# Kernel tuning notes

Measured on AMD Instinct MI355X. Metric: run time of the kernel, lower is better.

Reference implementation:

```python
import jax, jax.numpy as jnp
import numpy as np

NUM_EMBEDDINGS = 1024
EMBEDDING_SIZE = 256
COMMITMENT_COST = 0.25


def setup_inputs() -> dict:
    key = jax.random.key(0)
    kx, kw = jax.random.split(key)
    x = jax.random.normal(kx, (16, EMBEDDING_SIZE, 64, 64), dtype=jnp.float32)
    # nn.Embedding init: uniform(-1/K, 1/K)
    w = jax.random.uniform(kw, (NUM_EMBEDDINGS, EMBEDDING_SIZE), dtype=jnp.float32,
                           minval=-1.0 / NUM_EMBEDDINGS, maxval=1.0 / NUM_EMBEDDINGS)
    return {"x": x, "w": w}


def reference(x, w):
    # x: [B, C, H, W] -> NHWC
    xh = jnp.transpose(x, (0, 2, 3, 1))  # [B, H, W, D]
    B, H, W, D = xh.shape
    x_flat = xh.reshape(-1, D)  # [N, D]
    distances = (jnp.sum(x_flat * x_flat, axis=1, keepdims=True)
                 + jnp.sum(w * w, axis=1)
                 - 2.0 * (x_flat @ w.T))  # [N, K]
    indices_flat = jnp.argmin(distances, axis=1)  # [N]
    quantized = w[indices_flat].reshape(B, H, W, D)
    indices = indices_flat.reshape(B, H, W)[:, None, :, :]  # [B,1,H,W]
    # training-mode losses
    e_latent_loss = jnp.mean((jax.lax.stop_gradient(quantized) - xh) ** 2)
    q_latent_loss = jnp.mean((quantized - jax.lax.stop_gradient(xh)) ** 2)
    loss = q_latent_loss + COMMITMENT_COST * e_latent_loss
    # straight-through estimator
    quantized = xh + jax.lax.stop_gradient(quantized - xh)
    quantized = jnp.transpose(quantized, (0, 3, 1, 2))  # back to NCHW
    return quantized, indices, loss
```

## Files before the change

### kernel.cpp

```cpp
#include <hip/hip_runtime.h>
#include <math.h>

#define NUM_K 1024
#define DIM 256
#define HW 4096
#define NPIX 65536
#define QELEMS 16777216
#define MAX_FLAGS 16384

typedef short bf16x8 __attribute__((ext_vector_type(8)));
typedef float f32x4 __attribute__((ext_vector_type(4)));

__device__ __forceinline__ unsigned short f32_to_bf16_rne(float f) {
    unsigned int u = __float_as_uint(f);
    unsigned int r = u + 0x7FFFu + ((u >> 16) & 1u);
    return (unsigned short)(r >> 16);
}

__device__ __forceinline__ void merge3(float& a1d, int& a1i, float& a2d, int& a2i, float& a3d,
                                       float b1d, int b1i, float b2d, int b2i, float b3d) {
    bool bf = (b1d < a1d) || (b1d == a1d && b1i < a1i);
    float r1d = bf ? b1d : a1d; int r1i = bf ? b1i : a1i;
    float n2d = bf ? b2d : a2d; int n2i = bf ? b2i : a2i;
    float o1d = bf ? a1d : b1d; int o1i = bf ? a1i : b1i;
    bool k2 = (n2d < o1d) || (n2d == o1d && n2i < o1i);
    float r2d = k2 ? n2d : o1d; int r2i = k2 ? n2i : o1i;
    float sm3 = bf ? b3d : a3d;
    float o2d = bf ? a2d : b2d;
    float r3d = k2 ? fminf(sm3, o1d) : fminf(n2d, o2d);
    a1d = r1d; a1i = r1i; a2d = r2d; a2i = r2i; a3d = r3d;
}

__device__ __forceinline__ float np_sumsq_256(const float* __restrict__ p, long stride) {
    float blk0 = 0.f, blk1 = 0.f;
#pragma unroll
    for (int h = 0; h < 2; ++h) {
        const float* base = p + (long)h * 128 * stride;
        float s[16];
#pragma unroll
        for (int L = 0; L < 16; ++L) {
            float a0 = base[(long)(L)       * stride]; a0 = __fmul_rn(a0, a0);
            float a1 = base[(long)(16 + L)  * stride]; a1 = __fmul_rn(a1, a1);
            float a2 = base[(long)(32 + L)  * stride]; a2 = __fmul_rn(a2, a2);
            float a3 = base[(long)(48 + L)  * stride]; a3 = __fmul_rn(a3, a3);
            float a4 = base[(long)(64 + L)  * stride]; a4 = __fmul_rn(a4, a4);
            float a5 = base[(long)(80 + L)  * stride]; a5 = __fmul_rn(a5, a5);
            float a6 = base[(long)(96 + L)  * stride]; a6 = __fmul_rn(a6, a6);
            float a7 = base[(long)(112 + L) * stride]; a7 = __fmul_rn(a7, a7);
            float t1 = __fadd_rn(a0, a1);
            float t2 = __fadd_rn(a2, a3);
            float t3 = __fadd_rn(a4, a5);
            float t4 = __fadd_rn(a6, a7);
            s[L] = __fadd_rn(__fadd_rn(t1, t2), __fadd_rn(t3, t4));
        }
        float c0 = __fadd_rn(s[0], s[8]);
        float c1 = __fadd_rn(s[1], s[9]);
        float c2 = __fadd_rn(s[2], s[10]);
        float c3 = __fadd_rn(s[3], s[11]);
        float c4 = __fadd_rn(s[4], s[12]);
        float c5 = __fadd_rn(s[5], s[13]);
        float c6 = __fadd_rn(s[6], s[14]);
        float c7 = __fadd_rn(s[7], s[15]);
        float d0 = __fadd_rn(c0, c4);
        float d1 = __fadd_rn(c1, c5);
        float d2 = __fadd_rn(c2, c6);
        float d3 = __fadd_rn(c3, c7);
        float e0 = __fadd_rn(d0, d2);
        float e1 = __fadd_rn(d1, d3);
        float r  = __fadd_rn(e0, e1);
        if (h == 0) blk0 = r; else blk1 = r;
    }
    return __fadd_rn(blk0, blk1);
}

__global__ __launch_bounds__(256) void k_wsq(const float* __restrict__ w, float* __restrict__ wsq) {
    int k = blockIdx.x * 256 + threadIdx.x;
    if (k < NUM_K) wsq[k] = np_sumsq_256(w + (long)k * DIM, 1);
}

__global__ __launch_bounds__(256) void k_xsq(const float* __restrict__ x, float* __restrict__ xsq) {
    int n = blockIdx.x * 256 + threadIdx.x;
    int b = n >> 12, hw = n & 4095;
    xsq[n] = np_sumsq_256(x + (long)b * DIM * HW + hw, HW);
}

__global__ __launch_bounds__(1024)
void k_wtrans(const float* __restrict__ w, float* __restrict__ wtr) {
    int d = blockIdx.x;
    int k = threadIdx.x;
    wtr[(long)d * NUM_K + k] = w[(long)k * DIM + d];
}

__global__ __launch_bounds__(256)
void k_wfrag(const float* __restrict__ w, short* __restrict__ whi) {
    int id = blockIdx.x * 256 + threadIdx.x;
    int code = id >> 5;
    int c = id & 31;
    const float* src = w + (long)code * DIM + c * 8;
    bf16x8 vh;
#pragma unroll
    for (int j = 0; j < 8; ++j) vh[j] = (short)f32_to_bf16_rne(src[j]);
    int fl = ((c & 3) << 4) | (code & 15);
    long addr = ((((long)(code >> 4) * 8 + (c >> 2)) * 64 + fl) * 8);
    *(bf16x8*)(whi + addr) = vh;
}

#define A_SLOT(ks,m,fl) ((((ks)*4+(m))*64+(fl))*8)

__global__ __launch_bounds__(256, 2)
void k_argmin_mfma(const float* __restrict__ x,
                   const short* __restrict__ whi,
                   const float* __restrict__ wsq, float* __restrict__ xsq,
                   int* __restrict__ idx,
                   int4* __restrict__ pairf, int* __restrict__ paircnt,
                   int* __restrict__ fullf, int* __restrict__ fullcnt) {
    __shared__ short ahi[8 * 4 * 64 * 8];
    __shared__ float xpart[4 * 16 * 64];
    __shared__ float xsq_s[64];
    __shared__ float cd1[4][64], cd2[4][64], cd3[4][64];
    __shared__ int   ci1[4][64], ci2[4][64];

    const int t = threadIdx.x;
    const int lane = t & 63;
    const int q = t >> 6;
    const int tile = blockIdx.x;
    const int b = tile >> 6;
    const int hw0 = (tile & 63) * 64;
    const long px0 = (long)tile * 64;
    const float* xb = x + (long)b * (DIM * HW) + hw0 + lane;

    {
        float tmp[16], part[16];
#pragma unroll
        for (int i = 0; i < 8; ++i) {
            int c = q * 8 + i;
            float v[8];
#pragma unroll
            for (int jj = 0; jj < 8; ++jj) v[jj] = xb[(long)(c * 8 + jj) * HW];
            bf16x8 vh;
#pragma unroll
            for (int jj = 0; jj < 8; ++jj) vh[jj] = (short)f32_to_bf16_rne(v[jj]);
            int slot = A_SLOT(c >> 2, lane >> 4, ((c & 3) << 4) | (lane & 15));
            *(bf16x8*)(ahi + slot) = vh;
            const int kp = i >> 1;
#pragma unroll
            for (int jj = 0; jj < 8; ++jj) {
                int L = ((i & 1) << 3) | jj;
                float a = __fmul_rn(v[jj], v[jj]);
                if (kp == 0) tmp[L] = a;
                else if (kp == 1) part[L] = __fadd_rn(tmp[L], a);
                else if (kp == 2) tmp[L] = a;
                else part[L] = __fadd_rn(part[L], __fadd_rn(tmp[L], a));
            }
        }
#pragma unroll
        for (int L = 0; L < 16; ++L) xpart[(q * 16 + L) * 64 + lane] = part[L];
    }
    __syncthreads();

    if (t < 64) {
        float blk[2];
#pragma unroll
        for (int h = 0; h < 2; ++h) {
            float s[16];
#pragma unroll
            for (int L = 0; L < 16; ++L)
                s[L] = __fadd_rn(xpart[((2 * h) * 16 + L) * 64 + t],
                                 xpart[((2 * h + 1) * 16 + L) * 64 + t]);
            float c0 = __fadd_rn(s[0], s[8]);
            float c1 = __fadd_rn(s[1], s[9]);
            float c2 = __fadd_rn(s[2], s[10]);
            float c3 = __fadd_rn(s[3], s[11]);
            float c4 = __fadd_rn(s[4], s[12]);
            float c5 = __fadd_rn(s[5], s[13]);
            float c6 = __fadd_rn(s[6], s[14]);
            float c7 = __fadd_rn(s[7], s[15]);
            float d0 = __fadd_rn(c0, c4);
            float d1 = __fadd_rn(c1, c5);
            float d2 = __fadd_rn(c2, c6);
            float d3 = __fadd_rn(c3, c7);
            float e0 = __fadd_rn(d0, d2);
            float e1 = __fadd_rn(d1, d3);
            blk[h] = __fadd_rn(e0, e1);
        }
        float v = __fadd_rn(blk[0], blk[1]);
        xsq_s[t] = v;
        xsq[px0 + t] = v;
    }
    __syncthreads();

#pragma unroll
    for (int s = 0; s < 2; ++s) {
        const int ct0 = s * 32 + q * 8;
        f32x4 acc[4][8];
#pragma unroll
        for (int m = 0; m < 4; ++m)
#pragma unroll
            for (int n = 0; n < 8; ++n) acc[m][n] = (f32x4){0.f, 0.f, 0.f, 0.f};

#define BADDR(i) ((((long)(ct0 + ((i) & 7)) * 8 + ((i) >> 3)) * 64 + lane) * 8)
        bf16x8 bring[4];
#pragma unroll
        for (int i = 0; i < 4; ++i) bring[i] = *(const bf16x8*)(whi + BADDR(i));

        bf16x8 ah[4];
#pragma unroll
        for (int i = 0; i < 64; ++i) {
            const int ks = i >> 3;
            const int n = i & 7;
            if (n == 0) {
#pragma unroll
                for (int m = 0; m < 4; ++m)
                    ah[m] = *(const bf16x8*)(ahi + A_SLOT(ks, m, lane));
            }
            bf16x8 bcur = bring[i & 3];
            if (i + 4 < 64) bring[i & 3] = *(const bf16x8*)(whi + BADDR(i + 4));
#pragma unroll
            for (int m = 0; m < 4; ++m)
                acc[m][n] = __builtin_amdgcn_mfma_f32_16x16x32_bf16(ah[m], bcur, acc[m][n], 0, 0, 0);
        }
#undef BADDR

        const int rbase = (lane >> 4) * 4;
        float s1v[4][4];
#pragma unroll
        for (int m = 0; m < 4; ++m)
#pragma unroll
            for (int r = 0; r < 4; ++r) s1v[m][r] = xsq_s[16 * m + rbase + r];

        float e1d[4][4], e2d[4][4], e3d[4][4];
        int   e1i[4][4], e2i[4][4];
#pragma unroll
        for (int m = 0; m < 4; ++m)
#pragma unroll
            for (int r = 0; r < 4; ++r) {
                e1d[m][r] = INFINITY; e2d[m][r] = INFINITY; e3d[m][r] = INFINITY;
                e1i[m][r] = 0; e2i[m][r] = 0;
            }

#pragma unroll
        for (int n = 0; n < 8; ++n) {
            int code = (ct0 + n) * 16 + (lane & 15);
            float wq = wsq[code];
#pragma unroll
            for (int m = 0; m < 4; ++m) {
#pragma unroll
                for (int r = 0; r < 4; ++r) {
                    float tt = __fadd_rn(s1v[m][r], wq);
                    float dist = __fmaf_rn(-2.0f, acc[m][n][r], tt);
                    bool c1 = dist < e1d[m][r];
                    bool c2 = dist < e2d[m][r];
                    bool c3 = dist < e3d[m][r];
                    float n3 = c2 ? e2d[m][r] : (c3 ? dist : e3d[m][r]);
                    float n2 = c1 ? e1d[m][r] : (c2 ? dist : e2d[m][r]);
                    int   j2 = c1 ? e1i[m][r] : (c2 ? code : e2i[m][r]);
                    float n1 = c1 ? dist : e1d[m][r];
                    int   j1 = c1 ? code : e1i[m][r];
                    e3d[m][r] = n3; e2d[m][r] = n2; e2i[m][r] = j2;
                    e1d[m][r] = n1; e1i[m][r] = j1;
                }
            }
        }

#pragma unroll
        for (int step = 1; step < 16; step <<= 1) {
#pragma unroll
            for (int m = 0; m < 4; ++m) {
#pragma unroll
                for (int r = 0; r < 4; ++r) {
                    float o1 = __shfl_xor(e1d[m][r], step);
                    int   p1 = __shfl_xor(e1i[m][r], step);
                    float o2 = __shfl_xor(e2d[m][r], step);
                    int   p2 = __shfl_xor(e2i[m][r], step);
                    float o3 = __shfl_xor(e3d[m][r], step);
                    merge3(e1d[m][r], e1i[m][r], e2d[m][r], e2i[m][r], e3d[m][r],
                           o1, p1, o2, p2, o3);
                }
            }
        }

        if ((lane & 15) == 0) {
#pragma unroll
            for (int m = 0; m < 4; ++m) {
#pragma unroll
                for (int r = 0; r < 4; ++r) {
                    int px = 16 * m + rbase + r;
                    if (s == 0) {
                        cd1[q][px] = e1d[m][r]; ci1[q][px] = e1i[m][r];
                        cd2[q][px] = e2d[m][r]; ci2[q][px] = e2i[m][r];
                        cd3[q][px] = e3d[m][r];
                    } else {
                        float a1 = cd1[q][px], a2 = cd2[q][px], a3 = cd3[q][px];
                        int   ai = ci1[q][px], aj = ci2[q][px];
                        merge3(a1, ai, a2, aj, a3,
                               e1d[m][r], e1i[m][r], e2d[m][r], e2i[m][r], e3d[m][r]);
                        cd1[q][px] = a1; ci1[q][px] = ai;
                        cd2[q][px] = a2; ci2[q][px] = aj;
                        cd3[q][px] = a3;
                    }
                }
            }
        }
    }
    __syncthreads();

    if (t < 64) {
        float d1 = cd1[0][t], d2 = cd2[0][t], d3 = cd3[0][t];
        int   i1 = ci1[0][t], i2 = ci2[0][t];
#pragma unroll
        for (int sq = 1; sq < 4; ++sq) {
            merge3(d1, i1, d2, i2, d3,
                   cd1[sq][t], ci1[sq][t], cd2[sq][t], ci2[sq][t], cd3[sq][t]);
        }
        const long n = px0 + t;
        idx[n] = i1;
        float m = d1 * 2.5e-6f;
        if (__fsub_rn(d3, d1) <= m) {
            int pos = atomicAdd(fullcnt, 1);
            if (pos < MAX_FLAGS) fullf[pos] = (int)n;
        } else if (__fsub_rn(d2, d1) <= m) {
            int pos = atomicAdd(paircnt, 1);
            if (pos < MAX_FLAGS) pairf[pos] = (int4){(int)n, i1, i2, 0};
        }
    }
}

__global__ __launch_bounds__(256, 2)
void k_argmin_valu(const float* __restrict__ x, const float* __restrict__ w,
                   const float* __restrict__ wsq, const float* __restrict__ xsq,
                   int* __restrict__ idx, int* __restrict__ fullf, int* __restrict__ fullcnt) {
    __shared__ float xs[64 * 257];
    __shared__ float sd1[4][64];
    __shared__ float sd2[4][64];
    __shared__ int   si1[4][64];

    const int t = threadIdx.x;
    const int p = t & 63;
    const int q = t >> 6;
    const long n0 = (long)blockIdx.x * 64;
    const int b = (int)(n0 >> 12);
    const int hw0 = (int)(n0 & 4095);
    const float* xb = x + (long)b * DIM * HW + hw0;

    for (int i = 0; i < 64; ++i) {
        int c = q * 64 + i;
        xs[p * 257 + c] = xb[(long)c * HW + p];
    }
    __syncthreads();

    const float* xrow = xs + p * 257;
    const float s1 = xsq[n0 + p];
    float d1 = INFINITY, d2 = INFINITY;
    int i1 = 0;
    const int kbase = q * 256;
    const float* wq = w + (long)kbase * DIM;
    const float* wsq_q = wsq + kbase;

    for (int kc = 0; kc < 256; kc += 8) {
        float acc[8] = {0.f, 0.f, 0.f, 0.f, 0.f, 0.f, 0.f, 0.f};
        const float* w0 = wq + (long)kc * DIM;
#pragma unroll 2
        for (int d = 0; d < DIM; d += 4) {
            float x0 = xrow[d + 0];
            float x1 = xrow[d + 1];
            float x2 = xrow[d + 2];
            float x3 = xrow[d + 3];
#pragma unroll
            for (int j = 0; j < 8; ++j) {
                const float4 wv = *reinterpret_cast<const float4*>(w0 + j * DIM + d);
                acc[j] = __fmaf_rn(x0, wv.x, acc[j]);
                acc[j] = __fmaf_rn(x1, wv.y, acc[j]);
                acc[j] = __fmaf_rn(x2, wv.z, acc[j]);
                acc[j] = __fmaf_rn(x3, wv.w, acc[j]);
            }
        }
#pragma unroll
        for (int j = 0; j < 8; ++j) {
            float tk = __fadd_rn(s1, wsq_q[kc + j]);
            float dist = __fsub_rn(tk, __fmul_rn(2.0f, acc[j]));
            if (dist < d1) { d2 = d1; d1 = dist; i1 = kbase + kc + j; }
            else if (dist < d2) { d2 = dist; }
        }
    }

    sd1[q][p] = d1; sd2[q][p] = d2; si1[q][p] = i1;
    __syncthreads();
    if (q == 0) {
        float bd1 = sd1[0][p], bd2 = sd2[0][p];
        int bi = si1[0][p];
#pragma unroll
        for (int j = 1; j < 4; ++j) {
            float a1 = sd1[j][p], a2 = sd2[j][p];
            int ai = si1[j][p];
            if (a1 < bd1) { bd2 = fminf(bd1, a2); bd1 = a1; bi = ai; }
            else { bd2 = fminf(bd2, fminf(a1, a2)); }
        }
        const long n = n0 + p;
        idx[n] = bi;
        if (__fsub_rn(bd2, bd1) <= bd1 * 6.0e-7f) {
            int pos = atomicAdd(fullcnt, 1);
            if (pos < MAX_FLAGS) fullf[pos] = (int)n;
        }
    }
}

__global__ __launch_bounds__(256)
void k_refine_pair(const float* __restrict__ x, const float* __restrict__ w,
                   const float* __restrict__ wsq, const float* __restrict__ xsq,
                   const int4* __restrict__ pairf, const int* __restrict__ paircnt,
                   int* __restrict__ idx) {
    int np = *paircnt;
    if (np > MAX_FLAGS) np = MAX_FLAGS;
    const int lane = threadIdx.x & 63;
    const int wv = threadIdx.x >> 6;
    for (int fi = blockIdx.x * 4 + wv; fi < np; fi += gridDim.x * 4) {
        int4 f = pairf[fi];
        int n = f.x, c1 = f.y, c2 = f.z;
        int b = n >> 12, hw = n & 4095;
        const float* xp = x + (long)b * (DIM * HW) + hw;
        double xd0 = (double)xp[(long)(lane * 4 + 0) * HW];
        double xd1 = (double)xp[(long)(lane * 4 + 1) * HW];
        double xd2 = (double)xp[(long)(lane * 4 + 2) * HW];
        double xd3 = (double)xp[(long)(lane * 4 + 3) * HW];
        const float4 w1 = *reinterpret_cast<const float4*>(w + (long)c1 * DIM + lane * 4);
        const float4 w2 = *reinterpret_cast<const float4*>(w + (long)c2 * DIM + lane * 4);
        double s1 = fma((double)w1.x, xd0, fma((double)w1.y, xd1,
                    fma((double)w1.z, xd2, (double)w1.w * xd3)));
        double s2 = fma((double)w2.x, xd0, fma((double)w2.y, xd1,
                    fma((double)w2.z, xd2, (double)w2.w * xd3)));
#pragma unroll
        for (int st = 1; st < 64; st <<= 1) {
            s1 += __shfl_xor(s1, st);
            s2 += __shfl_xor(s2, st);
        }
        if (lane == 0) {
            float xq = xsq[n];
            float dk1 = __fsub_rn(__fadd_rn(xq, wsq[c1]), __fmul_rn(2.0f, (float)s1));
            float dk2 = __fsub_rn(__fadd_rn(xq, wsq[c2]), __fmul_rn(2.0f, (float)s2));
            bool take2 = (dk2 < dk1) || (dk2 == dk1 && c2 < c1);
            idx[n] = take2 ? c2 : c1;
        }
    }
}

__global__ __launch_bounds__(1024)
void k_refine_full(const float* __restrict__ x, const float* __restrict__ wtr,
                   const float* __restrict__ wsq, const float* __restrict__ xsq,
                   const int* __restrict__ fullf, const int* __restrict__ fullcnt,
                   int* __restrict__ idx) {
    __shared__ float xsf[DIM][8];
    __shared__ int   np_s[8];
    __shared__ float s1_s[8];
    __shared__ float wd[16][8];
    __shared__ int   wi[16][8];

    int nf = *fullcnt;
    if (nf > MAX_FLAGS) nf = MAX_FLAGS;
    const int t = threadIdx.x;
    const int lane = t & 63;
    const int wid = t >> 6;

    for (int base = blockIdx.x * 8; base < nf; base += gridDim.x * 8) {
        __syncthreads();
        if (t < 8) {
            int fi = base + t;
            int n = fullf[fi < nf ? fi : (nf - 1)];
            np_s[t] = n;
            s1_s[t] = xsq[n];
        }
        __syncthreads();
#pragma unroll
        for (int e = t; e < 2048; e += 1024) {
            int p = e & 7, d = e >> 3;
            int n = np_s[p];
            xsf[d][p] = x[(long)(n >> 12) * (DIM * HW) + (long)d * HW + (n & 4095)];
        }
        __syncthreads();

        const float wq = wsq[t];
        double acc[8] = {0.0, 0.0, 0.0, 0.0, 0.0, 0.0, 0.0, 0.0};
#pragma unroll 4
        for (int d = 0; d < DIM; ++d) {
            double wk = (double)wtr[(long)d * NUM_K + t];
#pragma unroll
            for (int p = 0; p < 8; ++p) acc[p] = fma(wk, (double)xsf[d][p], acc[p]);
        }

        float dkv[8];
        int   kiv[8];
#pragma unroll
        for (int p = 0; p < 8; ++p) {
            dkv[p] = __fsub_rn(__fadd_rn(s1_s[p], wq), __fmul_rn(2.0f, (float)acc[p]));
            kiv[p] = t;
        }
#pragma unroll
        for (int step = 1; step < 64; step <<= 1) {
#pragma unroll
            for (int p = 0; p < 8; ++p) {
                float od = __shfl_xor(dkv[p], step);
                int   oi = __shfl_xor(kiv[p], step);
                if (od < dkv[p] || (od == dkv[p] && oi < kiv[p])) { dkv[p] = od; kiv[p] = oi; }
            }
        }
        if (lane == 0) {
#pragma unroll
            for (int p = 0; p < 8; ++p) { wd[wid][p] = dkv[p]; wi[wid][p] = kiv[p]; }
        }
        __syncthreads();
        if (t < 8) {
            float bd = wd[0][t];
            int   bi = wi[0][t];
#pragma unroll
            for (int sq = 1; sq < 16; ++sq) {
                float ad = wd[sq][t];
                int   ai = wi[sq][t];
                if (ad < bd || (ad == bd && ai < bi)) { bd = ad; bi = ai; }
            }
            if (base + t < nf) idx[np_s[t]] = bi;
        }
    }
}

__global__ __launch_bounds__(256, 2)
void k_quant(const float* __restrict__ x, const float* __restrict__ w,
             const int* __restrict__ idx, float* __restrict__ qout,
             float* __restrict__ iout, float* __restrict__ loss) {
    __shared__ float wrow[64 * 257];
    __shared__ int lidx[64];
    __shared__ float part[4];
    const int t = threadIdx.x;
    const long n0 = (long)blockIdx.x * 64;
    const int b = (int)(n0 >> 12), hw0 = (int)(n0 & 4095);

    if (t < 64) lidx[t] = idx[n0 + t];
    __syncthreads();
    for (int i = 0; i < 64; ++i) {
        wrow[i * 257 + t] = w[(long)lidx[i] * DIM + t];
    }
    if (t < 64) iout[n0 + t] = (float)lidx[t];
    __syncthreads();

    const int p = t & 63, cg = t >> 6;
    const float* xb = x + (long)b * DIM * HW + hw0;
    float* qb = qout + (long)b * DIM * HW + hw0;
    float lsum = 0.f;
    for (int i = 0; i < 64; ++i) {
        int c = cg * 64 + i;
        float qv = wrow[p * 257 + c];
        long off = (long)c * HW + p;
        float xv = xb[off];
        float diff = __fsub_rn(qv, xv);
        qb[off] = __fadd_rn(xv, diff);
        lsum = __fmaf_rn(diff, diff, lsum);
    }
#pragma unroll
    for (int off = 32; off; off >>= 1) lsum += __shfl_down(lsum, off);
    if ((t & 63) == 0) part[t >> 6] = lsum;
    __syncthreads();
    if (t == 0) {
        float tot = (part[0] + part[1]) + (part[2] + part[3]);
        atomicAdd(loss, tot * (1.25f / 16777216.f));
    }
}

extern "C" void kernel_launch(void* const* d_in, const int* in_sizes, int n_in,
                              void* d_out, int out_size, void* d_ws, size_t ws_size,
                              hipStream_t stream) {
    const float* x = (const float*)d_in[0];
    const float* w = (const float*)d_in[1];

    float* qout = (float*)d_out;
    float* iout = qout + QELEMS;
    float* loss = iout + NPIX;

    char* wp = (char*)d_ws;
    int*   idx     = (int*)wp;      wp += (size_t)NPIX * 4;
    float* wsq     = (float*)wp;    wp += (size_t)NUM_K * 4;
    float* xsq     = (float*)wp;    wp += (size_t)NPIX * 4;
    int4*  pairf   = (int4*)wp;     wp += (size_t)MAX_FLAGS * 16;
    int*   paircnt = (int*)wp;      wp += 256;
    int*   fullf   = (int*)wp;      wp += (size_t)MAX_FLAGS * 4;
    int*   fullcnt = (int*)wp;      wp += 256;
    float* wtr     = (float*)wp;    wp += (size_t)NUM_K * DIM * 4;
    short* whi     = (short*)wp;    wp += (size_t)NUM_K * DIM * 2;
    size_t need = (size_t)(wp - (char*)d_ws);

    hipMemsetAsync(loss, 0, sizeof(float), stream);
    hipMemsetAsync(paircnt, 0, sizeof(int), stream);
    hipMemsetAsync(fullcnt, 0, sizeof(int), stream);

    k_wsq<<<4, 256, 0, stream>>>(w, wsq);
    k_wtrans<<<DIM, 1024, 0, stream>>>(w, wtr);

    if (ws_size >= need) {
        k_wfrag<<<128, 256, 0, stream>>>(w, whi);
        k_argmin_mfma<<<1024, 256, 0, stream>>>(x, whi, wsq, xsq, idx,
                                                pairf, paircnt, fullf, fullcnt);
        k_refine_pair<<<2048, 256, 0, stream>>>(x, w, wsq, xsq, pairf, paircnt, idx);
    } else {
        k_xsq<<<NPIX / 256, 256, 0, stream>>>(x, xsq);
        k_argmin_valu<<<NPIX / 64, 256, 0, stream>>>(x, w, wsq, xsq, idx, fullf, fullcnt);
    }
    k_refine_full<<<512, 1024, 0, stream>>>(x, wtr, wsq, xsq, fullf, fullcnt, idx);
    k_quant<<<NPIX / 64, 256, 0, stream>>>(x, w, idx, qout, iout, loss);
}
```

Baseline: 239.7 us.

## Fuse codebook prep kernels and memsets; keep top-3 across both MFMA passes

```diff
diff --git a/kernel.cpp b/kernel.cpp
--- a/kernel.cpp
+++ b/kernel.cpp
@@ -73,36 +73,45 @@
     return __fadd_rn(blk0, blk1);
 }
 
-__global__ __launch_bounds__(256) void k_wsq(const float* __restrict__ w, float* __restrict__ wsq) {
-    int k = blockIdx.x * 256 + threadIdx.x;
-    if (k < NUM_K) wsq[k] = np_sumsq_256(w + (long)k * DIM, 1);
+__global__ __launch_bounds__(256)
+void k_prep(const float* __restrict__ w, float* __restrict__ wsq,
+            float* __restrict__ wtr, short* __restrict__ whi,
+            float* __restrict__ loss, int* __restrict__ paircnt, int* __restrict__ fullcnt) {
+    const int bk = blockIdx.x;
+    const int t = threadIdx.x;
+    if (bk < 128) {
+        int id = bk * 256 + t;
+        int code = id >> 5;
+        int c = id & 31;
+        const float* src = w + (long)code * DIM + c * 8;
+        bf16x8 vh;
+#pragma unroll
+        for (int j = 0; j < 8; ++j) vh[j] = (short)f32_to_bf16_rne(src[j]);
+        int fl = ((c & 3) << 4) | (code & 15);
+        long addr = ((((long)(code >> 4) * 8 + (c >> 2)) * 64 + fl) * 8);
+        *(bf16x8*)(whi + addr) = vh;
+    } else if (bk < 256) {
+        int d0 = (bk - 128) * 2;
+#pragma unroll
+        for (int dd = 0; dd < 2; ++dd) {
+            int d = d0 + dd;
+#pragma unroll
+            for (int kk = 0; kk < 4; ++kk) {
+                int k = kk * 256 + t;
+                wtr[(long)d * NUM_K + k] = w[(long)k * DIM + d];
+            }
+        }
+    } else {
+        int k = (bk - 256) * 256 + t;
+        wsq[k] = np_sumsq_256(w + (long)k * DIM, 1);
+        if (bk == 256 && t == 0) { *loss = 0.f; *paircnt = 0; *fullcnt = 0; }
+    }
 }
 
 __global__ __launch_bounds__(256) void k_xsq(const float* __restrict__ x, float* __restrict__ xsq) {
     int n = blockIdx.x * 256 + threadIdx.x;
     int b = n >> 12, hw = n & 4095;
     xsq[n] = np_sumsq_256(x + (long)b * DIM * HW + hw, HW);
-}
-
-__global__ __launch_bounds__(1024)
-void k_wtrans(const float* __restrict__ w, float* __restrict__ wtr) {
-    int d = blockIdx.x;
-    int k = threadIdx.x;
-    wtr[(long)d * NUM_K + k] = w[(long)k * DIM + d];
-}
-
-__global__ __launch_bounds__(256)
-void k_wfrag(const float* __restrict__ w, short* __restrict__ whi) {
-    int id = blockIdx.x * 256 + threadIdx.x;
-    int code = id >> 5;
-    int c = id & 31;
-    const float* src = w + (long)code * DIM + c * 8;
-    bf16x8 vh;
-#pragma unroll
-    for (int j = 0; j < 8; ++j) vh[j] = (short)f32_to_bf16_rne(src[j]);
-    int fl = ((c & 3) << 4) | (code & 15);
-    long addr = ((((long)(code >> 4) * 8 + (c >> 2)) * 64 + fl) * 8);
-    *(bf16x8*)(whi + addr) = vh;
 }
 
 #define A_SLOT(ks,m,fl) ((((ks)*4+(m))*64+(fl))*8)
@@ -189,6 +198,23 @@
     }
     __syncthreads();
 
+    const int rbase = (lane >> 4) * 4;
+    float s1v[4][4];
+#pragma unroll
+    for (int m = 0; m < 4; ++m)
+#pragma unroll
+        for (int r = 0; r < 4; ++r) s1v[m][r] = xsq_s[16 * m + rbase + r];
+
+    float e1d[4][4], e2d[4][4], e3d[4][4];
+    int   e1i[4][4], e2i[4][4];
+#pragma unroll
+    for (int m = 0; m < 4; ++m)
+#pragma unroll
+        for (int r = 0; r < 4; ++r) {
+            e1d[m][r] = INFINITY; e2d[m][r] = INFINITY; e3d[m][r] = INFINITY;
+            e1i[m][r] = 0; e2i[m][r] = 0;
+        }
+
 #pragma unroll
     for (int s = 0; s < 2; ++s) {
         const int ct0 = s * 32 + q * 8;
@@ -220,23 +246,6 @@
                 acc[m][n] = __builtin_amdgcn_mfma_f32_16x16x32_bf16(ah[m], bcur, acc[m][n], 0, 0, 0);
         }
 #undef BADDR
-
-        const int rbase = (lane >> 4) * 4;
-        float s1v[4][4];
-#pragma unroll
-        for (int m = 0; m < 4; ++m)
-#pragma unroll
-            for (int r = 0; r < 4; ++r) s1v[m][r] = xsq_s[16 * m + rbase + r];
-
-        float e1d[4][4], e2d[4][4], e3d[4][4];
-        int   e1i[4][4], e2i[4][4];
-#pragma unroll
-        for (int m = 0; m < 4; ++m)
-#pragma unroll
-            for (int r = 0; r < 4; ++r) {
-                e1d[m][r] = INFINITY; e2d[m][r] = INFINITY; e3d[m][r] = INFINITY;
-                e1i[m][r] = 0; e2i[m][r] = 0;
-            }
 
 #pragma unroll
         for (int n = 0; n < 8; ++n) {
@@ -261,44 +270,34 @@
                 }
             }
         }
-
-#pragma unroll
-        for (int step = 1; step < 16; step <<= 1) {
-#pragma unroll
-            for (int m = 0; m < 4; ++m) {
-#pragma unroll
-                for (int r = 0; r < 4; ++r) {
-                    float o1 = __shfl_xor(e1d[m][r], step);
-                    int   p1 = __shfl_xor(e1i[m][r], step);
-                    float o2 = __shfl_xor(e2d[m][r], step);
-                    int   p2 = __shfl_xor(e2i[m][r], step);
-                    float o3 = __shfl_xor(e3d[m][r], step);
-                    merge3(e1d[m][r], e1i[m][r], e2d[m][r], e2i[m][r], e3d[m][r],
-                           o1, p1, o2, p2, o3);
-                }
-            }
-        }
-
-        if ((lane & 15) == 0) {
-#pragma unroll
-            for (int m = 0; m < 4; ++m) {
-#pragma unroll
-                for (int r = 0; r < 4; ++r) {
-                    int px = 16 * m + rbase + r;
-                    if (s == 0) {
-                        cd1[q][px] = e1d[m][r]; ci1[q][px] = e1i[m][r];
-                        cd2[q][px] = e2d[m][r]; ci2[q][px] = e2i[m][r];
-                        cd3[q][px] = e3d[m][r];
-                    } else {
-                        float a1 = cd1[q][px], a2 = cd2[q][px], a3 = cd3[q][px];
-                        int   ai = ci1[q][px], aj = ci2[q][px];
-                        merge3(a1, ai, a2, aj, a3,
-                               e1d[m][r], e1i[m][r], e2d[m][r], e2i[m][r], e3d[m][r]);
-                        cd1[q][px] = a1; ci1[q][px] = ai;
-                        cd2[q][px] = a2; ci2[q][px] = aj;
-                        cd3[q][px] = a3;
-                    }
-                }
+    }
+
+#pragma unroll
+    for (int step = 1; step < 16; step <<= 1) {
+#pragma unroll
+        for (int m = 0; m < 4; ++m) {
+#pragma unroll
+            for (int r = 0; r < 4; ++r) {
+                float o1 = __shfl_xor(e1d[m][r], step);
+                int   p1 = __shfl_xor(e1i[m][r], step);
+                float o2 = __shfl_xor(e2d[m][r], step);
+                int   p2 = __shfl_xor(e2i[m][r], step);
+                float o3 = __shfl_xor(e3d[m][r], step);
+                merge3(e1d[m][r], e1i[m][r], e2d[m][r], e2i[m][r], e3d[m][r],
+                       o1, p1, o2, p2, o3);
+            }
+        }
+    }
+
+    if ((lane & 15) == 0) {
+#pragma unroll
+        for (int m = 0; m < 4; ++m) {
+#pragma unroll
+            for (int r = 0; r < 4; ++r) {
+                int px = 16 * m + rbase + r;
+                cd1[q][px] = e1d[m][r]; ci1[q][px] = e1i[m][r];
+                cd2[q][px] = e2d[m][r]; ci2[q][px] = e2i[m][r];
+                cd3[q][px] = e3d[m][r];
             }
         }
     }
@@ -585,15 +584,9 @@
     short* whi     = (short*)wp;    wp += (size_t)NUM_K * DIM * 2;
     size_t need = (size_t)(wp - (char*)d_ws);
 
-    hipMemsetAsync(loss, 0, sizeof(float), stream);
-    hipMemsetAsync(paircnt, 0, sizeof(int), stream);
-    hipMemsetAsync(fullcnt, 0, sizeof(int), stream);
-
-    k_wsq<<<4, 256, 0, stream>>>(w, wsq);
-    k_wtrans<<<DIM, 1024, 0, stream>>>(w, wtr);
+    k_prep<<<260, 256, 0, stream>>>(w, wsq, wtr, whi, loss, paircnt, fullcnt);
 
     if (ws_size >= need) {
-        k_wfrag<<<128, 256, 0, stream>>>(w, whi);
         k_argmin_mfma<<<1024, 256, 0, stream>>>(x, whi, wsq, xsq, idx,
                                                 pairf, paircnt, fullf, fullcnt);
         k_refine_pair<<<2048, 256, 0, stream>>>(x, w, wsq, xsq, pairf, paircnt, idx);
```

New measurement: 418.8 us. 1.75x slower.
